# Performance work log

Measured on AMD Instinct MI355X. Metric: run time of the kernel, lower is better.

## Reference

```python
import jax, jax.numpy as jnp
import numpy as np

EPS = 1e-6
ALPHA = 0.2  # LeakyReLU negative slope


def layer_norm(x, g, b):
    mu = jnp.mean(x, axis=-1, keepdims=True)
    var = jnp.mean(jnp.square(x - mu), axis=-1, keepdims=True)
    return (x - mu) * jax.lax.rsqrt(var + EPS) * g + b


def graph_attention(x, bias, W, a_src, a_dst):
    # x: [B,N,D], bias: [B,N,N], W: [D, H*Dh], a_src/a_dst: [H, Dh]
    B, N, D = x.shape
    H, Dh = a_src.shape
    h = jnp.einsum('bnd,dhk->bhnk', x, W.reshape(D, H, Dh))  # [B,H,N,Dh]
    s = jnp.einsum('bhnk,hk->bhn', h, a_src)                 # source term
    t = jnp.einsum('bhnk,hk->bhn', h, a_dst)                 # target term
    e = jax.nn.leaky_relu(s[:, :, :, None] + t[:, :, None, :], ALPHA)
    e = e + bias[:, None, :, :]                              # graph mask/bias
    attn = jax.nn.softmax(e, axis=-1)                        # [B,H,N,N]
    out = jnp.einsum('bhij,bhjk->bhik', attn, h)             # [B,H,N,Dh]
    return out.transpose(0, 2, 1, 3).reshape(B, N, H * Dh)


def setup_inputs() -> dict:
    key = jax.random.key(0)
    ks = jax.random.split(key, 8)
    B, N, D, H = 2, 2048, 512, 8
    Dh = D // H
    sc = 1.0 / np.sqrt(D)
    return {
        'x': jax.random.normal(ks[0], (B, N, D), jnp.float32),
        'bias': jax.random.normal(ks[1], (B, N, N), jnp.float32),
        'W1': jax.random.normal(ks[2], (D, D), jnp.float32) * sc,
        'a_src1': jax.random.normal(ks[3], (H, Dh), jnp.float32) * sc,
        'a_dst1': jax.random.normal(ks[4], (H, Dh), jnp.float32) * sc,
        'g1': jnp.ones((D,), jnp.float32),
        'b1': jnp.zeros((D,), jnp.float32),
        'W2': jax.random.normal(ks[5], (D, D), jnp.float32) * sc,
        'a_src2': jax.random.normal(ks[6], (1, D), jnp.float32) * sc,
        'a_dst2': jax.random.normal(ks[7], (1, D), jnp.float32) * sc,
        'g2': jnp.ones((D,), jnp.float32),
        'b2': jnp.zeros((D,), jnp.float32),
    }


def reference(x, bias, W1, a_src1, a_dst1, g1, b1, W2, a_src2, a_dst2, g2, b2):
    # dropout is identity in eval mode
    attn_in = layer_norm(x, g1, b1)
    attn = graph_attention(attn_in, bias, W1, a_src1, a_dst1) + x
    attn_in2 = layer_norm(attn, g2, b2)
    out = graph_attention(attn_in2, bias, W2, a_src2, a_dst2) + attn
    return out
```

## Files before the change

kernel.cpp:

```cpp
#include <hip/hip_runtime.h>
#include <math.h>

#define NB 2
#define NN 2048
#define DD 512
#define L2E 1.44269504088896340736f

typedef __attribute__((ext_vector_type(8))) short short8;
typedef __attribute__((ext_vector_type(4))) float f32x4;

__device__ __forceinline__ unsigned short f2bf(float x) {
  union { float f; unsigned u; } a;
  a.f = x;
  unsigned r = a.u + 0x7FFF + ((a.u >> 16) & 1);
  return (unsigned short)(r >> 16);
}
__device__ __forceinline__ float bf2f(unsigned short u) {
  union { unsigned u; float f; } a;
  a.u = ((unsigned)u) << 16;
  return a.f;
}
__device__ __forceinline__ unsigned cvtpk(float lo, float hi) {
  unsigned r;
  asm("v_cvt_pk_bf16_f32 %0, %1, %2" : "=v"(r) : "v"(lo), "v"(hi));
  return r;
}
__device__ __forceinline__ uint2 exp4pk(float e0, float e1, float e2, float e3) {
  float p0, p1, p2, p3;
  uint2 d;
  asm("v_exp_f32 %2, %6\n\t"
      "v_exp_f32 %3, %7\n\t"
      "v_exp_f32 %4, %8\n\t"
      "v_exp_f32 %5, %9\n\t"
      "v_cvt_pk_bf16_f32 %0, %2, %3\n\t"
      "v_cvt_pk_bf16_f32 %1, %4, %5"
      : "=&v"(d.x), "=&v"(d.y), "=&v"(p0), "=&v"(p1), "=&v"(p2), "=&v"(p3)
      : "v"(e0), "v"(e1), "v"(e2), "v"(e3));
  return d;
}

__device__ __forceinline__ float waveReduceSum(float v) {
#pragma unroll
  for (int o = 32; o; o >>= 1) v += __shfl_down(v, o, 64);
  return v;
}
__device__ __forceinline__ float blockReduceSum(float v, float* red4) {
  int tid = threadIdx.x;
  __syncthreads();
  v = waveReduceSum(v);
  if ((tid & 63) == 0) red4[tid >> 6] = v;
  __syncthreads();
  return red4[0] + red4[1] + red4[2] + red4[3];
}

__global__ __launch_bounds__(256) void prep_kernel(
    const float* __restrict__ W1, const float* __restrict__ W2,
    unsigned short* __restrict__ WT1, unsigned short* __restrict__ WT2,
    const float* __restrict__ as1, const float* __restrict__ ad1,
    float* __restrict__ vs1, float* __restrict__ vd1,
    const float* __restrict__ as2, const float* __restrict__ ad2,
    float* __restrict__ vs2, float* __restrict__ vd2) {
  __shared__ float tile[64][65];
  int bid = blockIdx.x;
  int t = threadIdx.x;
  if (bid < 128) {
    const float* W = (bid & 64) ? W2 : W1;
    unsigned short* WT = (bid & 64) ? WT2 : WT1;
    int r = bid & 63;
    int kt = (r >> 3) * 64, ct = (r & 7) * 64;
#pragma unroll
    for (int u = 0; u < 16; u++) {
      int lin = t + u * 256;
      int kl = lin >> 6, cl = lin & 63;
      tile[kl][cl] = W[(size_t)(kt + kl) * DD + ct + cl];
    }
    __syncthreads();
#pragma unroll
    for (int u = 0; u < 16; u++) {
      int lin = t + u * 256;
      int cl = lin >> 6, kl = lin & 63;
      WT[(size_t)(ct + cl) * DD + kt + kl] = f2bf(tile[kl][cl]);
    }
  } else {
    int idx = bid - 128;
    int slot = idx >> 3, dch = idx & 7;
    const float *W, *as, *ad;
    float *vs, *vd;
    int Dh, hoff;
    if (slot < 8) {
      W = W1; as = as1 + slot * 64; ad = ad1 + slot * 64;
      vs = vs1 + (size_t)slot * DD; vd = vd1 + (size_t)slot * DD;
      Dh = 64; hoff = slot * 64;
    } else {
      W = W2; as = as2; ad = ad2; vs = vs2; vd = vd2;
      Dh = 512; hoff = 0;
    }
    int dl = t >> 2, kq = t & 3;
    int d = dch * 64 + dl;
    int kn = Dh >> 2;
    const float* wr = W + (size_t)d * DD + hoff + kq * kn;
    const float* asp = as + kq * kn;
    const float* adp = ad + kq * kn;
    float s = 0.f, dd2 = 0.f;
    for (int k = 0; k < kn; k++) {
      float wv = wr[k];
      s += wv * asp[k];
      dd2 += wv * adp[k];
    }
    s += __shfl_xor(s, 1);
    s += __shfl_xor(s, 2);
    dd2 += __shfl_xor(dd2, 1);
    dd2 += __shfl_xor(dd2, 2);
    if (kq == 0) {
      vs[d] = s;
      vd[d] = dd2;
    }
  }
}

__global__ __launch_bounds__(256) void lnst_kernel(
    const float* __restrict__ x, const float* __restrict__ g,
    const float* __restrict__ bb, unsigned short* __restrict__ y,
    const float* __restrict__ vs, const float* __restrict__ vd,
    float* __restrict__ sOut, float* __restrict__ tOut, int HN) {
  __shared__ float red4[4];
  __shared__ float lnS[512];
  int row = blockIdx.x;
  int t = threadIdx.x;
  const float* xr = x + (size_t)row * DD;
  float2 v = *(const float2*)&xr[2 * t];
  float s = blockReduceSum(v.x + v.y, red4);
  float mu = s * (1.0f / 512.0f);
  float d0 = v.x - mu, d1 = v.y - mu;
  float ss = blockReduceSum(d0 * d0 + d1 * d1, red4);
  float rstd = rsqrtf(ss * (1.0f / 512.0f) + 1e-6f);
  float2 gg = *(const float2*)&g[2 * t];
  float2 bv = *(const float2*)&bb[2 * t];
  float n0 = d0 * rstd * gg.x + bv.x;
  float n1 = d1 * rstd * gg.y + bv.y;
  ushort2 o;
  o.x = f2bf(n0);
  o.y = f2bf(n1);
  *(ushort2*)&y[(size_t)row * DD + 2 * t] = o;
  lnS[2 * t] = n0;
  lnS[2 * t + 1] = n1;
  __syncthreads();
  int wv = t >> 6, l = t & 63;
  int b = row >> 11, n = row & (NN - 1);
  float4 x0 = *(const float4*)&lnS[l * 8];
  float4 x1 = *(const float4*)&lnS[l * 8 + 4];
  for (int h = wv; h < HN; h += 4) {
    const float* vsr = vs + (size_t)h * DD + l * 8;
    const float* vdr = vd + (size_t)h * DD + l * 8;
    float4 a0 = *(const float4*)vsr, a1 = *(const float4*)(vsr + 4);
    float4 c0 = *(const float4*)vdr, c1 = *(const float4*)(vdr + 4);
    float ps = x0.x * a0.x + x0.y * a0.y + x0.z * a0.z + x0.w * a0.w +
               x1.x * a1.x + x1.y * a1.y + x1.z * a1.z + x1.w * a1.w;
    float pd = x0.x * c0.x + x0.y * c0.y + x0.z * c0.z + x0.w * c0.w +
               x1.x * c1.x + x1.y * c1.y + x1.z * c1.z + x1.w * c1.w;
#pragma unroll
    for (int o2 = 32; o2; o2 >>= 1) {
      ps += __shfl_xor(ps, o2);
      pd += __shfl_xor(pd, o2);
    }
    if (l == 0) {
      sOut[((size_t)b * HN + h) * NN + n] = ps * L2E;
      tOut[((size_t)b * HN + h) * NN + n] = pd * L2E;
    }
  }
}

__global__ __launch_bounds__(256) void gemm_kernel(const unsigned short* __restrict__ A,
                                                   const unsigned short* __restrict__ BT,
                                                   unsigned short* __restrict__ hbT) {
  __shared__ float accL[4][16][65];
  int t = threadIdx.x, w = t >> 6, l = t & 63;
  int li = l & 15, lg = l >> 4;
  int R0 = blockIdx.x * 16;
  int c0 = blockIdx.y * 64;
  const unsigned short* ar = A + (size_t)(R0 + li) * DD + w * 128 + lg * 8;
  const unsigned short* br = BT + (size_t)(c0 + li) * DD + w * 128 + lg * 8;
  f32x4 acc[4] = {};
#pragma unroll
  for (int k0 = 0; k0 < 128; k0 += 32) {
    short8 af = *(const short8*)(ar + k0);
#pragma unroll
    for (int f = 0; f < 4; f++) {
      short8 bf = *(const short8*)(br + (size_t)f * 16 * DD + k0);
      acc[f] = __builtin_amdgcn_mfma_f32_16x16x32_bf16(af, bf, acc[f], 0, 0, 0);
    }
  }
#pragma unroll
  for (int f = 0; f < 4; f++)
#pragma unroll
    for (int r = 0; r < 4; r++) accL[w][lg * 4 + r][f * 16 + li] = acc[f][r];
  __syncthreads();
  int b = R0 >> 11, jT = (R0 & (NN - 1)) >> 4;
#pragma unroll
  for (int u = 0; u < 2; u++) {
    int idx = t + u * 256;
    int f = idx >> 7;
    int rem = idx & 127;
    int cl = rem >> 3, jlp = rem & 7;
    int cc = f * 16 + cl;
    float v0 = accL[0][2 * jlp][cc] + accL[1][2 * jlp][cc] + accL[2][2 * jlp][cc] +
               accL[3][2 * jlp][cc];
    float v1 = accL[0][2 * jlp + 1][cc] + accL[1][2 * jlp + 1][cc] +
               accL[2][2 * jlp + 1][cc] + accL[3][2 * jlp + 1][cc];
    size_t off = (((size_t)(b * (DD / 64) + blockIdx.y) * (NN / 16)) + jT) * 1024 +
                 f * 256 + cl * 16 + jlp * 2;
    *(unsigned*)(hbT + off) = cvtpk(v0, v1);
  }
}

__global__ __launch_bounds__(512) void pvh_kernel(
    const unsigned short* __restrict__ hbT, const float* __restrict__ bias,
    const float* __restrict__ sArr, const float* __restrict__ tArr,
    const float* __restrict__ res, float* __restrict__ out) {
  __shared__ unsigned short Pl[8][2][1024];
  int t = threadIdx.x, w = t >> 6, l = t & 63;
  int li = l & 15, lg = l >> 4;
  int i0g = blockIdx.x * 16;
  int b = i0g >> 11, i0 = i0g & (NN - 1);
  size_t bhN = (size_t)(b * 8 + w) * NN;
  const float* trow = tArr + bhN;

  int rs = l >> 3, js = (l & 7) * 8, jc = l & 7;
  int wchunk = ((jc & 4) | ((jc & 3) ^ (rs & 3))) * 8;
  float sv[2];
  sv[0] = sArr[bhN + i0 + rs];
  sv[1] = sArr[bhN + i0 + 8 + rs];
  const float* bb0 = bias + ((size_t)b * NN + i0 + rs) * NN;
  const float* bb1 = bb0 + (size_t)8 * NN;

  const unsigned short* vbase =
      hbT + ((size_t)(b * 8 + w) * (NN / 16)) * 1024 + (lg >> 1) * 1024 + li * 16 +
      (lg & 1) * 8;
  int ra0 = li * 64 + (lg ^ (li & 3)) * 8;
  int ra1 = ra0 + 32;

  union { short8 v; unsigned short q[8]; } ones;
#pragma unroll
  for (int k = 0; k < 8; k++) ones.q[k] = 0x3F80;

  f32x4 acc[4] = {};
  f32x4 accS = {0.f, 0.f, 0.f, 0.f};

  auto loadTB = [&](int j, float4& t0, float4& t1, float4& b0a, float4& b0b,
                    float4& b1a, float4& b1b) {
    t0 = *(const float4*)&trow[j + js];
    t1 = *(const float4*)&trow[j + js + 4];
    b0a = *(const float4*)&bb0[j + js];
    b0b = *(const float4*)&bb0[j + js + 4];
    b1a = *(const float4*)&bb1[j + js];
    b1b = *(const float4*)&bb1[j + js + 4];
  };
  auto computeP = [&](const float4& t0, const float4& t1, const float4& b0a,
                      const float4& b0b, const float4& b1a, const float4& b1b, int pb) {
#pragma unroll
    for (int u = 0; u < 2; u++) {
      const float4& ba = u ? b1a : b0a;
      const float4& bc = u ? b1b : b0b;
      int row = u * 8 + rs;
      float e0 = sv[u] + t0.x, e1 = sv[u] + t0.y;
      float e2 = sv[u] + t0.z, e3 = sv[u] + t0.w;
      float e4 = sv[u] + t1.x, e5 = sv[u] + t1.y;
      float e6 = sv[u] + t1.z, e7 = sv[u] + t1.w;
      e0 = fmaf(ba.x, L2E, fmaxf(e0, 0.2f * e0));
      e1 = fmaf(ba.y, L2E, fmaxf(e1, 0.2f * e1));
      e2 = fmaf(ba.z, L2E, fmaxf(e2, 0.2f * e2));
      e3 = fmaf(ba.w, L2E, fmaxf(e3, 0.2f * e3));
      e4 = fmaf(bc.x, L2E, fmaxf(e4, 0.2f * e4));
      e5 = fmaf(bc.y, L2E, fmaxf(e5, 0.2f * e5));
      e6 = fmaf(bc.z, L2E, fmaxf(e6, 0.2f * e6));
      e7 = fmaf(bc.w, L2E, fmaxf(e7, 0.2f * e7));
      uint2 d0 = exp4pk(e0, e1, e2, e3);
      uint2 d1 = exp4pk(e4, e5, e6, e7);
      uint4 dd;
      dd.x = d0.x; dd.y = d0.y; dd.z = d1.x; dd.w = d1.y;
      *(uint4*)&Pl[w][pb][row * 64 + wchunk] = dd;
    }
  };

  float4 tA0, tA1, bA0, bA1, bA2, bA3;

  loadTB(0, tA0, tA1, bA0, bA1, bA2, bA3);
  computeP(tA0, tA1, bA0, bA1, bA2, bA3, 0);
  loadTB(64, tA0, tA1, bA0, bA1, bA2, bA3);

  int buf = 0;
  for (int jt = 0; jt < NN; jt += 64) {
    const unsigned short* vp = vbase + (size_t)jt * 64;
    short8 v0 = *(const short8*)(vp + 0);
    short8 v1 = *(const short8*)(vp + 256);
    short8 v2 = *(const short8*)(vp + 512);
    short8 v3 = *(const short8*)(vp + 768);
    short8 v4 = *(const short8*)(vp + 2048);
    short8 v5 = *(const short8*)(vp + 2304);
    short8 v6 = *(const short8*)(vp + 2560);
    short8 v7 = *(const short8*)(vp + 2816);
    short8 a0 = *(const short8*)&Pl[w][buf][ra0];
    short8 a1 = *(const short8*)&Pl[w][buf][ra1];
    if (jt + 64 < NN) {
      float4 n0 = tA0, n1 = tA1, m0 = bA0, m1 = bA1, m2 = bA2, m3 = bA3;
      int jn = (jt + 128 < NN) ? (jt + 128) : 0;
      loadTB(jn, tA0, tA1, bA0, bA1, bA2, bA3);
      computeP(n0, n1, m0, m1, m2, m3, buf ^ 1);
    }
    __builtin_amdgcn_s_setprio(1);
    accS = __builtin_amdgcn_mfma_f32_16x16x32_bf16(a0, ones.v, accS, 0, 0, 0);
    acc[0] = __builtin_amdgcn_mfma_f32_16x16x32_bf16(a0, v0, acc[0], 0, 0, 0);
    acc[1] = __builtin_amdgcn_mfma_f32_16x16x32_bf16(a0, v1, acc[1], 0, 0, 0);
    acc[2] = __builtin_amdgcn_mfma_f32_16x16x32_bf16(a0, v2, acc[2], 0, 0, 0);
    acc[3] = __builtin_amdgcn_mfma_f32_16x16x32_bf16(a0, v3, acc[3], 0, 0, 0);
    accS = __builtin_amdgcn_mfma_f32_16x16x32_bf16(a1, ones.v, accS, 0, 0, 0);
    acc[0] = __builtin_amdgcn_mfma_f32_16x16x32_bf16(a1, v4, acc[0], 0, 0, 0);
    acc[1] = __builtin_amdgcn_mfma_f32_16x16x32_bf16(a1, v5, acc[1], 0, 0, 0);
    acc[2] = __builtin_amdgcn_mfma_f32_16x16x32_bf16(a1, v6, acc[2], 0, 0, 0);
    acc[3] = __builtin_amdgcn_mfma_f32_16x16x32_bf16(a1, v7, acc[3], 0, 0, 0);
    __builtin_amdgcn_s_setprio(0);
    buf ^= 1;
  }

#pragma unroll
  for (int r = 0; r < 4; r++) {
    float inv = 1.0f / accS[r];
    size_t ix = ((size_t)b * NN + i0 + lg * 4 + r) * DD + w * 64 + li;
#pragma unroll
    for (int f = 0; f < 4; f++) out[ix + f * 16] = acc[f][r] * inv + res[ix + f * 16];
  }
}

template <int HN, int CCH>
__global__ __launch_bounds__(256) void pv_kernel(
    const unsigned short* __restrict__ hbT, const float* __restrict__ bias,
    const float* __restrict__ sArr, const float* __restrict__ tArr,
    const float* __restrict__ res, float* __restrict__ out) {
  constexpr int DH = DD / HN;
  __shared__ unsigned short Pl[4][2][1024];
  __shared__ float accL[4][16][33];
  __shared__ float sLa[4][16];
  int t = threadIdx.x, w = t >> 6, l = t & 63;
  int li = l & 15, lg = l >> 4;
  int i0 = blockIdx.x * 16;
  int ck = blockIdx.y, bh = blockIdx.z;
  int h = bh % HN, b = bh / HN;
  int c0 = h * DH + ck * (CCH * 64);
  size_t bhN = (size_t)bh * NN;
  const float* trow = tArr + bhN;

  int rs = l >> 3, js = (l & 7) * 8, jc = l & 7;
  int wchunk = ((jc & 4) | ((jc & 3) ^ (rs & 3))) * 8;
  float sv[2];
  sv[0] = sArr[bhN + i0 + rs];
  sv[1] = sArr[bhN + i0 + 8 + rs];
  const float* bb0 = bias + ((size_t)b * NN + i0 + rs) * NN;
  const float* bb1 = bb0 + (size_t)8 * NN;

  const unsigned short* vbase =
      hbT + ((size_t)(b * (DD / 64) + (c0 >> 6)) * (NN / 16)) * 1024 +
      (lg >> 1) * 1024 + li * 16 + (lg & 1) * 8;
  int ra0 = li * 64 + (lg ^ (li & 3)) * 8;
  int ra1 = ra0 + 32;

  union { short8 v; unsigned short q[8]; } ones;
#pragma unroll
  for (int k = 0; k < 8; k++) ones.q[k] = 0x3F80;

  const int jbeg = w * (NN / 4), jend = jbeg + NN / 4;
  f32x4 acc[CCH][4] = {};
  f32x4 accS = {0.f, 0.f, 0.f, 0.f};

  auto loadTB = [&](int j, float4& t0, float4& t1, float4& b0a, float4& b0b,
                    float4& b1a, float4& b1b) {
    t0 = *(const float4*)&trow[j + js];
    t1 = *(const float4*)&trow[j + js + 4];
    b0a = *(const float4*)&bb0[j + js];
    b0b = *(const float4*)&bb0[j + js + 4];
    b1a = *(const float4*)&bb1[j + js];
    b1b = *(const float4*)&bb1[j + js + 4];
  };
  auto computeP = [&](const float4& t0, const float4& t1, const float4& b0a,
                      const float4& b0b, const float4& b1a, const float4& b1b, int pb) {
#pragma unroll
    for (int u = 0; u < 2; u++) {
      const float4& ba = u ? b1a : b0a;
      const float4& bc = u ? b1b : b0b;
      int row = u * 8 + rs;
      float e0 = sv[u] + t0.x, e1 = sv[u] + t0.y;
      float e2 = sv[u] + t0.z, e3 = sv[u] + t0.w;
      float e4 = sv[u] + t1.x, e5 = sv[u] + t1.y;
      float e6 = sv[u] + t1.z, e7 = sv[u] + t1.w;
      e0 = fmaf(ba.x, L2E, fmaxf(e0, 0.2f * e0));
      e1 = fmaf(ba.y, L2E, fmaxf(e1, 0.2f * e1));
      e2 = fmaf(ba.z, L2E, fmaxf(e2, 0.2f * e2));
      e3 = fmaf(ba.w, L2E, fmaxf(e3, 0.2f * e3));
      e4 = fmaf(bc.x, L2E, fmaxf(e4, 0.2f * e4));
      e5 = fmaf(bc.y, L2E, fmaxf(e5, 0.2f * e5));
      e6 = fmaf(bc.z, L2E, fmaxf(e6, 0.2f * e6));
      e7 = fmaf(bc.w, L2E, fmaxf(e7, 0.2f * e7));
      uint2 d0 = exp4pk(e0, e1, e2, e3);
      uint2 d1 = exp4pk(e4, e5, e6, e7);
      uint4 dd;
      dd.x = d0.x; dd.y = d0.y; dd.z = d1.x; dd.w = d1.y;
      *(uint4*)&Pl[w][pb][row * 64 + wchunk] = dd;
    }
  };

  float4 tA0, tA1, bA0, bA1, bA2, bA3;

  loadTB(jbeg, tA0, tA1, bA0, bA1, bA2, bA3);
  computeP(tA0, tA1, bA0, bA1, bA2, bA3, 0);
  loadTB(jbeg + 64, tA0, tA1, bA0, bA1, bA2, bA3);

  int buf = 0;
  for (int jt = jbeg; jt < jend; jt += 64) {
    short8 a0 = *(const short8*)&Pl[w][buf][ra0];
    short8 a1 = *(const short8*)&Pl[w][buf][ra1];
    if (jt + 64 < jend) {
      float4 n0 = tA0, n1 = tA1, m0 = bA0, m1 = bA1, m2 = bA2, m3 = bA3;
      int jn = (jt + 128 < jend) ? (jt + 128) : jbeg;
      loadTB(jn, tA0, tA1, bA0, bA1, bA2, bA3);
      computeP(n0, n1, m0, m1, m2, m3, buf ^ 1);
    }
    __builtin_amdgcn_s_setprio(1);
    accS = __builtin_amdgcn_mfma_f32_16x16x32_bf16(a0, ones.v, accS, 0, 0, 0);
    accS = __builtin_amdgcn_mfma_f32_16x16x32_bf16(a1, ones.v, accS, 0, 0, 0);
#pragma unroll
    for (int cc = 0; cc < CCH; cc++) {
      const unsigned short* vp =
          vbase + (size_t)cc * ((NN / 16) * 1024) + (size_t)jt * 64;
      short8 v0 = *(const short8*)(vp + 0);
      short8 v1 = *(const short8*)(vp + 256);
      short8 v2 = *(const short8*)(vp + 512);
      short8 v3 = *(const short8*)(vp + 768);
      acc[cc][0] = __builtin_amdgcn_mfma_f32_16x16x32_bf16(a0, v0, acc[cc][0], 0, 0, 0);
      acc[cc][1] = __builtin_amdgcn_mfma_f32_16x16x32_bf16(a0, v1, acc[cc][1], 0, 0, 0);
      acc[cc][2] = __builtin_amdgcn_mfma_f32_16x16x32_bf16(a0, v2, acc[cc][2], 0, 0, 0);
      acc[cc][3] = __builtin_amdgcn_mfma_f32_16x16x32_bf16(a0, v3, acc[cc][3], 0, 0, 0);
      short8 v4 = *(const short8*)(vp + 2048);
      short8 v5 = *(const short8*)(vp + 2304);
      short8 v6 = *(const short8*)(vp + 2560);
      short8 v7 = *(const short8*)(vp + 2816);
      acc[cc][0] = __builtin_amdgcn_mfma_f32_16x16x32_bf16(a1, v4, acc[cc][0], 0, 0, 0);
      acc[cc][1] = __builtin_amdgcn_mfma_f32_16x16x32_bf16(a1, v5, acc[cc][1], 0, 0, 0);
      acc[cc][2] = __builtin_amdgcn_mfma_f32_16x16x32_bf16(a1, v6, acc[cc][2], 0, 0, 0);
      acc[cc][3] = __builtin_amdgcn_mfma_f32_16x16x32_bf16(a1, v7, acc[cc][3], 0, 0, 0);
    }
    __builtin_amdgcn_s_setprio(0);
    buf ^= 1;
  }

  if (li == 0) {
#pragma unroll
    for (int r = 0; r < 4; r++) sLa[w][lg * 4 + r] = accS[r];
  }
#pragma unroll
  for (int g = 0; g < 2 * CCH; g++) {
    int cc = g >> 1, half = g & 1;
#pragma unroll
    for (int f = 0; f < 2; f++)
#pragma unroll
      for (int r = 0; r < 4; r++)
        accL[w][lg * 4 + r][f * 16 + li] = acc[cc][half * 2 + f][r];
    __syncthreads();
    {
      int rr = t >> 4, cp = (t & 15) * 2;
      float S = sLa[0][rr] + sLa[1][rr] + sLa[2][rr] + sLa[3][rr];
      float inv = 1.0f / S;
      float2 O = {0.f, 0.f};
#pragma unroll
      for (int w2 = 0; w2 < 4; w2++) {
        O.x += accL[w2][rr][cp];
        O.y += accL[w2][rr][cp + 1];
      }
      size_t ix = ((size_t)b * NN + i0 + rr) * DD + c0 + cc * 64 + half * 32 + cp;
      float2 rv = *(const float2*)&res[ix];
      float2 ov = {O.x * inv + rv.x, O.y * inv + rv.y};
      *(float2*)&out[ix] = ov;
    }
    __syncthreads();
  }
}

extern "C" void kernel_launch(void* const* d_in, const int* in_sizes, int n_in,
                              void* d_out, int out_size, void* d_ws, size_t ws_size,
                              hipStream_t stream) {
  const float* x = (const float*)d_in[0];
  const float* bias = (const float*)d_in[1];
  const float* W1 = (const float*)d_in[2];
  const float* asrc1 = (const float*)d_in[3];
  const float* adst1 = (const float*)d_in[4];
  const float* g1 = (const float*)d_in[5];
  const float* b1 = (const float*)d_in[6];
  const float* W2 = (const float*)d_in[7];
  const float* asrc2 = (const float*)d_in[8];
  const float* adst2 = (const float*)d_in[9];
  const float* g2 = (const float*)d_in[10];
  const float* b2 = (const float*)d_in[11];
  float* out = (float*)d_out;
  float* ws = (float*)d_ws;

  const size_t RC = (size_t)NB * NN * DD;
  float* attnBuf = ws;
  unsigned short* lnB = (unsigned short*)(ws + RC);
  unsigned short* hbT = (unsigned short*)(ws + RC + RC / 2);
  unsigned short* WT1 = (unsigned short*)(ws + 2 * RC);
  unsigned short* WT2 = WT1 + (size_t)DD * DD;
  float* vs1 = (float*)(WT2 + (size_t)DD * DD);
  float* vd1 = vs1 + 8 * DD;
  float* vs2 = vd1 + 8 * DD;
  float* vd2 = vs2 + DD;
  float* sBuf = vd2 + DD;
  float* tBuf = sBuf + 16 * NN;

  const int rows = NB * NN;

  hipLaunchKernelGGL(prep_kernel, dim3(128 + 72), dim3(256), 0, stream, W1, W2, WT1, WT2,
                     asrc1, adst1, vs1, vd1, asrc2, adst2, vs2, vd2);

  hipLaunchKernelGGL(lnst_kernel, dim3(rows), dim3(256), 0, stream, x, g1, b1, lnB, vs1, vd1,
                     sBuf, tBuf, 8);
  hipLaunchKernelGGL(gemm_kernel, dim3(256, 8), dim3(256), 0, stream, lnB, WT1, hbT);
  hipLaunchKernelGGL(pvh_kernel, dim3(256), dim3(512), 0, stream, hbT, bias, sBuf, tBuf, x,
                     attnBuf);

  hipLaunchKernelGGL(lnst_kernel, dim3(rows), dim3(256), 0, stream, attnBuf, g2, b2, lnB, vs2,
                     vd2, sBuf, tBuf, 1);
  hipLaunchKernelGGL(gemm_kernel, dim3(256, 8), dim3(256), 0, stream, lnB, WT2, hbT);
  hipLaunchKernelGGL((pv_kernel<1, 4>), dim3(128, 2, 2), dim3(256), 0, stream, hbT, bias,
                     sBuf, tBuf, attnBuf, out);
}
```

Baseline: 160.3 us.

## Split pvh key range across two wave groups with LDS merge

The multi-head attention-times-V kernel now launches 1024 threads per block, with two groups of 8 waves each handling half of the key dimension for every head. Partial output accumulators and softmax denominators from the second half are written to shared memory and added by the first half before normalization and the residual add. This doubles the resident waves per block to give more latency hiding on a 256-block grid, at the cost of a 64KB shared buffer, two barriers, and the register limit imposed by 1024-thread blocks. The P tile layout in LDS is also changed to a row-split indexing.

```diff
diff --git a/kernel.cpp b/kernel.cpp
--- a/kernel.cpp
+++ b/kernel.cpp
@@ -213,16 +213,18 @@
   }
 }
 
-__global__ __launch_bounds__(512) void pvh_kernel(
+__global__ __launch_bounds__(1024) void pvh_kernel(
     const unsigned short* __restrict__ hbT, const float* __restrict__ bias,
     const float* __restrict__ sArr, const float* __restrict__ tArr,
     const float* __restrict__ res, float* __restrict__ out) {
-  __shared__ unsigned short Pl[8][2][1024];
+  __shared__ __align__(16) unsigned char smem[65536];
+  unsigned short (*Pl)[2][1024] = (unsigned short (*)[2][1024])smem;
   int t = threadIdx.x, w = t >> 6, l = t & 63;
+  int h = w & 7, jh = w >> 3;
   int li = l & 15, lg = l >> 4;
   int i0g = blockIdx.x * 16;
   int b = i0g >> 11, i0 = i0g & (NN - 1);
-  size_t bhN = (size_t)(b * 8 + w) * NN;
+  size_t bhN = (size_t)(b * 8 + h) * NN;
   const float* trow = tArr + bhN;
 
   int rs = l >> 3, js = (l & 7) * 8, jc = l & 7;
@@ -234,7 +236,7 @@
   const float* bb1 = bb0 + (size_t)8 * NN;
 
   const unsigned short* vbase =
-      hbT + ((size_t)(b * 8 + w) * (NN / 16)) * 1024 + (lg >> 1) * 1024 + li * 16 +
+      hbT + ((size_t)(b * 8 + h) * (NN / 16)) * 1024 + (lg >> 1) * 1024 + li * 16 +
       (lg & 1) * 8;
   int ra0 = li * 64 + (lg ^ (li & 3)) * 8;
   int ra1 = ra0 + 32;
@@ -244,6 +246,155 @@
   for (int k = 0; k < 8; k++) ones.q[k] = 0x3F80;
 
   f32x4 acc[4] = {};
+  f32x4 accS = {0.f, 0.f, 0.f, 0.f};
+
+  auto loadTB = [&](int j, float4& t0, float4& t1, float4& b0a, float4& b0b,
+                    float4& b1a, float4& b1b) {
+    t0 = *(const float4*)&trow[j + js];
+    t1 = *(const float4*)&trow[j + js + 4];
+    b0a = *(const float4*)&bb0[j + js];
+    b0b = *(const float4*)&bb0[j + js + 4];
+    b1a = *(const float4*)&bb1[j + js];
+    b1b = *(const float4*)&bb1[j + js + 4];
+  };
+  auto computeP = [&](const float4& t0, const float4& t1, const float4& b0a,
+                      const float4& b0b, const float4& b1a, const float4& b1b, int pb) {
+#pragma unroll
+    for (int u = 0; u < 2; u++) {
+      const float4& ba = u ? b1a : b0a;
+      const float4& bc = u ? b1b : b0b;
+      int row = u * 8 + rs;
+      float e0 = sv[u] + t0.x, e1 = sv[u] + t0.y;
+      float e2 = sv[u] + t0.z, e3 = sv[u] + t0.w;
+      float e4 = sv[u] + t1.x, e5 = sv[u] + t1.y;
+      float e6 = sv[u] + t1.z, e7 = sv[u] + t1.w;
+      e0 = fmaf(ba.x, L2E, fmaxf(e0, 0.2f * e0));
+      e1 = fmaf(ba.y, L2E, fmaxf(e1, 0.2f * e1));
+      e2 = fmaf(ba.z, L2E, fmaxf(e2, 0.2f * e2));
+      e3 = fmaf(ba.w, L2E, fmaxf(e3, 0.2f * e3));
+      e4 = fmaf(bc.x, L2E, fmaxf(e4, 0.2f * e4));
+      e5 = fmaf(bc.y, L2E, fmaxf(e5, 0.2f * e5));
+      e6 = fmaf(bc.z, L2E, fmaxf(e6, 0.2f * e6));
+      e7 = fmaf(bc.w, L2E, fmaxf(e7, 0.2f * e7));
+      uint2 d0 = exp4pk(e0, e1, e2, e3);
+      uint2 d1 = exp4pk(e4, e5, e6, e7);
+      uint4 dd;
+      dd.x = d0.x; dd.y = d0.y; dd.z = d1.x; dd.w = d1.y;
+      *(uint4*)&Pl[w][pb][rs * 64 + u * 512 + wchunk] = dd;
+    }
+  };
+
+  const int jbeg = jh * (NN / 2), jend = jbeg + NN / 2;
+  float4 tA0, tA1, bA0, bA1, bA2, bA3;
+
+  loadTB(jbeg, tA0, tA1, bA0, bA1, bA2, bA3);
+  computeP(tA0, tA1, bA0, bA1, bA2, bA3, 0);
+  loadTB(jbeg + 64, tA0, tA1, bA0, bA1, bA2, bA3);
+
+  int buf = 0;
+  for (int jt = jbeg; jt < jend; jt += 64) {
+    const unsigned short* vp = vbase + (size_t)jt * 64;
+    short8 v0 = *(const short8*)(vp + 0);
+    short8 v1 = *(const short8*)(vp + 256);
+    short8 v2 = *(const short8*)(vp + 512);
+    short8 v3 = *(const short8*)(vp + 768);
+    short8 v4 = *(const short8*)(vp + 2048);
+    short8 v5 = *(const short8*)(vp + 2304);
+    short8 v6 = *(const short8*)(vp + 2560);
+    short8 v7 = *(const short8*)(vp + 2816);
+    short8 a0 = *(const short8*)&Pl[w][buf][(li & 7) * 64 + (li >> 3) * 512 +
+                                            ((lg ^ (li & 3)) * 8)];
+    short8 a1 = *(const short8*)&Pl[w][buf][(li & 7) * 64 + (li >> 3) * 512 + 32 +
+                                            ((lg ^ (li & 3)) * 8)];
+    if (jt + 64 < jend) {
+      float4 n0 = tA0, n1 = tA1, m0 = bA0, m1 = bA1, m2 = bA2, m3 = bA3;
+      int jn = (jt + 128 < jend) ? (jt + 128) : jbeg;
+      loadTB(jn, tA0, tA1, bA0, bA1, bA2, bA3);
+      computeP(n0, n1, m0, m1, m2, m3, buf ^ 1);
+    }
+    __builtin_amdgcn_s_setprio(1);
+    accS = __builtin_amdgcn_mfma_f32_16x16x32_bf16(a0, ones.v, accS, 0, 0, 0);
+    acc[0] = __builtin_amdgcn_mfma_f32_16x16x32_bf16(a0, v0, acc[0], 0, 0, 0);
+    acc[1] = __builtin_amdgcn_mfma_f32_16x16x32_bf16(a0, v1, acc[1], 0, 0, 0);
+    acc[2] = __builtin_amdgcn_mfma_f32_16x16x32_bf16(a0, v2, acc[2], 0, 0, 0);
+    acc[3] = __builtin_amdgcn_mfma_f32_16x16x32_bf16(a0, v3, acc[3], 0, 0, 0);
+    accS = __builtin_amdgcn_mfma_f32_16x16x32_bf16(a1, ones.v, accS, 0, 0, 0);
+    acc[0] = __builtin_amdgcn_mfma_f32_16x16x32_bf16(a1, v4, acc[0], 0, 0, 0);
+    acc[1] = __builtin_amdgcn_mfma_f32_16x16x32_bf16(a1, v5, acc[1], 0, 0, 0);
+    acc[2] = __builtin_amdgcn_mfma_f32_16x16x32_bf16(a1, v6, acc[2], 0, 0, 0);
+    acc[3] = __builtin_amdgcn_mfma_f32_16x16x32_bf16(a1, v7, acc[3], 0, 0, 0);
+    __builtin_amdgcn_s_setprio(0);
+    buf ^= 1;
+  }
+
+  __syncthreads();
+  float* mAcc = (float*)smem;
+  float* mS = (float*)(smem + 8 * 16 * 68 * 4);
+  if (jh == 1) {
+#pragma unroll
+    for (int f = 0; f < 4; f++)
+#pragma unroll
+      for (int r = 0; r < 4; r++)
+        mAcc[((size_t)h * 16 + lg * 4 + r) * 68 + f * 16 + li] = acc[f][r];
+    if (li == 0) {
+#pragma unroll
+      for (int r = 0; r < 4; r++) mS[h * 16 + lg * 4 + r] = accS[r];
+    }
+  }
+  __syncthreads();
+  if (jh == 0) {
+#pragma unroll
+    for (int r = 0; r < 4; r++) {
+      float S = accS[r] + mS[h * 16 + lg * 4 + r];
+      float inv = 1.0f / S;
+      size_t ix = ((size_t)b * NN + i0 + lg * 4 + r) * DD + h * 64 + li;
+#pragma unroll
+      for (int f = 0; f < 4; f++) {
+        float O = acc[f][r] + mAcc[((size_t)h * 16 + lg * 4 + r) * 68 + f * 16 + li];
+        out[ix + f * 16] = O * inv + res[ix + f * 16];
+      }
+    }
+  }
+}
+
+template <int HN, int CCH>
+__global__ __launch_bounds__(256) void pv_kernel(
+    const unsigned short* __restrict__ hbT, const float* __restrict__ bias,
+    const float* __restrict__ sArr, const float* __restrict__ tArr,
+    const float* __restrict__ res, float* __restrict__ out) {
+  constexpr int DH = DD / HN;
+  __shared__ unsigned short Pl[4][2][1024];
+  __shared__ float accL[4][16][33];
+  __shared__ float sLa[4][16];
+  int t = threadIdx.x, w = t >> 6, l = t & 63;
+  int li = l & 15, lg = l >> 4;
+  int i0 = blockIdx.x * 16;
+  int ck = blockIdx.y, bh = blockIdx.z;
+  int h = bh % HN, b = bh / HN;
+  int c0 = h * DH + ck * (CCH * 64);
+  size_t bhN = (size_t)bh * NN;
+  const float* trow = tArr + bhN;
+
+  int rs = l >> 3, js = (l & 7) * 8, jc = l & 7;
+  int wchunk = ((jc & 4) | ((jc & 3) ^ (rs & 3))) * 8;
+  float sv[2];
+  sv[0] = sArr[bhN + i0 + rs];
+  sv[1] = sArr[bhN + i0 + 8 + rs];
+  const float* bb0 = bias + ((size_t)b * NN + i0 + rs) * NN;
+  const float* bb1 = bb0 + (size_t)8 * NN;
+
+  const unsigned short* vbase =
+      hbT + ((size_t)(b * (DD / 64) + (c0 >> 6)) * (NN / 16)) * 1024 +
+      (lg >> 1) * 1024 + li * 16 + (lg & 1) * 8;
+  int ra0 = li * 64 + (lg ^ (li & 3)) * 8;
+  int ra1 = ra0 + 32;
+
+  union { short8 v; unsigned short q[8]; } ones;
+#pragma unroll
+  for (int k = 0; k < 8; k++) ones.q[k] = 0x3F80;
+
+  const int jbeg = w * (NN / 4), jend = jbeg + NN / 4;
+  f32x4 acc[CCH][4] = {};
   f32x4 accS = {0.f, 0.f, 0.f, 0.f};
 
   auto loadTB = [&](int j, float4& t0, float4& t1, float4& b0a, float4& b0b,
@@ -284,131 +435,6 @@
 
   float4 tA0, tA1, bA0, bA1, bA2, bA3;
 
-  loadTB(0, tA0, tA1, bA0, bA1, bA2, bA3);
-  computeP(tA0, tA1, bA0, bA1, bA2, bA3, 0);
-  loadTB(64, tA0, tA1, bA0, bA1, bA2, bA3);
-
-  int buf = 0;
-  for (int jt = 0; jt < NN; jt += 64) {
-    const unsigned short* vp = vbase + (size_t)jt * 64;
-    short8 v0 = *(const short8*)(vp + 0);
-    short8 v1 = *(const short8*)(vp + 256);
-    short8 v2 = *(const short8*)(vp + 512);
-    short8 v3 = *(const short8*)(vp + 768);
-    short8 v4 = *(const short8*)(vp + 2048);
-    short8 v5 = *(const short8*)(vp + 2304);
-    short8 v6 = *(const short8*)(vp + 2560);
-    short8 v7 = *(const short8*)(vp + 2816);
-    short8 a0 = *(const short8*)&Pl[w][buf][ra0];
-    short8 a1 = *(const short8*)&Pl[w][buf][ra1];
-    if (jt + 64 < NN) {
-      float4 n0 = tA0, n1 = tA1, m0 = bA0, m1 = bA1, m2 = bA2, m3 = bA3;
-      int jn = (jt + 128 < NN) ? (jt + 128) : 0;
-      loadTB(jn, tA0, tA1, bA0, bA1, bA2, bA3);
-      computeP(n0, n1, m0, m1, m2, m3, buf ^ 1);
-    }
-    __builtin_amdgcn_s_setprio(1);
-    accS = __builtin_amdgcn_mfma_f32_16x16x32_bf16(a0, ones.v, accS, 0, 0, 0);
-    acc[0] = __builtin_amdgcn_mfma_f32_16x16x32_bf16(a0, v0, acc[0], 0, 0, 0);
-    acc[1] = __builtin_amdgcn_mfma_f32_16x16x32_bf16(a0, v1, acc[1], 0, 0, 0);
-    acc[2] = __builtin_amdgcn_mfma_f32_16x16x32_bf16(a0, v2, acc[2], 0, 0, 0);
-    acc[3] = __builtin_amdgcn_mfma_f32_16x16x32_bf16(a0, v3, acc[3], 0, 0, 0);
-    accS = __builtin_amdgcn_mfma_f32_16x16x32_bf16(a1, ones.v, accS, 0, 0, 0);
-    acc[0] = __builtin_amdgcn_mfma_f32_16x16x32_bf16(a1, v4, acc[0], 0, 0, 0);
-    acc[1] = __builtin_amdgcn_mfma_f32_16x16x32_bf16(a1, v5, acc[1], 0, 0, 0);
-    acc[2] = __builtin_amdgcn_mfma_f32_16x16x32_bf16(a1, v6, acc[2], 0, 0, 0);
-    acc[3] = __builtin_amdgcn_mfma_f32_16x16x32_bf16(a1, v7, acc[3], 0, 0, 0);
-    __builtin_amdgcn_s_setprio(0);
-    buf ^= 1;
-  }
-
-#pragma unroll
-  for (int r = 0; r < 4; r++) {
-    float inv = 1.0f / accS[r];
-    size_t ix = ((size_t)b * NN + i0 + lg * 4 + r) * DD + w * 64 + li;
-#pragma unroll
-    for (int f = 0; f < 4; f++) out[ix + f * 16] = acc[f][r] * inv + res[ix + f * 16];
-  }
-}
-
-template <int HN, int CCH>
-__global__ __launch_bounds__(256) void pv_kernel(
-    const unsigned short* __restrict__ hbT, const float* __restrict__ bias,
-    const float* __restrict__ sArr, const float* __restrict__ tArr,
-    const float* __restrict__ res, float* __restrict__ out) {
-  constexpr int DH = DD / HN;
-  __shared__ unsigned short Pl[4][2][1024];
-  __shared__ float accL[4][16][33];
-  __shared__ float sLa[4][16];
-  int t = threadIdx.x, w = t >> 6, l = t & 63;
-  int li = l & 15, lg = l >> 4;
-  int i0 = blockIdx.x * 16;
-  int ck = blockIdx.y, bh = blockIdx.z;
-  int h = bh % HN, b = bh / HN;
-  int c0 = h * DH + ck * (CCH * 64);
-  size_t bhN = (size_t)bh * NN;
-  const float* trow = tArr + bhN;
-
-  int rs = l >> 3, js = (l & 7) * 8, jc = l & 7;
-  int wchunk = ((jc & 4) | ((jc & 3) ^ (rs & 3))) * 8;
-  float sv[2];
-  sv[0] = sArr[bhN + i0 + rs];
-  sv[1] = sArr[bhN + i0 + 8 + rs];
-  const float* bb0 = bias + ((size_t)b * NN + i0 + rs) * NN;
-  const float* bb1 = bb0 + (size_t)8 * NN;
-
-  const unsigned short* vbase =
-      hbT + ((size_t)(b * (DD / 64) + (c0 >> 6)) * (NN / 16)) * 1024 +
-      (lg >> 1) * 1024 + li * 16 + (lg & 1) * 8;
-  int ra0 = li * 64 + (lg ^ (li & 3)) * 8;
-  int ra1 = ra0 + 32;
-
-  union { short8 v; unsigned short q[8]; } ones;
-#pragma unroll
-  for (int k = 0; k < 8; k++) ones.q[k] = 0x3F80;
-
-  const int jbeg = w * (NN / 4), jend = jbeg + NN / 4;
-  f32x4 acc[CCH][4] = {};
-  f32x4 accS = {0.f, 0.f, 0.f, 0.f};
-
-  auto loadTB = [&](int j, float4& t0, float4& t1, float4& b0a, float4& b0b,
-                    float4& b1a, float4& b1b) {
-    t0 = *(const float4*)&trow[j + js];
-    t1 = *(const float4*)&trow[j + js + 4];
-    b0a = *(const float4*)&bb0[j + js];
-    b0b = *(const float4*)&bb0[j + js + 4];
-    b1a = *(const float4*)&bb1[j + js];
-    b1b = *(const float4*)&bb1[j + js + 4];
-  };
-  auto computeP = [&](const float4& t0, const float4& t1, const float4& b0a,
-                      const float4& b0b, const float4& b1a, const float4& b1b, int pb) {
-#pragma unroll
-    for (int u = 0; u < 2; u++) {
-      const float4& ba = u ? b1a : b0a;
-      const float4& bc = u ? b1b : b0b;
-      int row = u * 8 + rs;
-      float e0 = sv[u] + t0.x, e1 = sv[u] + t0.y;
-      float e2 = sv[u] + t0.z, e3 = sv[u] + t0.w;
-      float e4 = sv[u] + t1.x, e5 = sv[u] + t1.y;
-      float e6 = sv[u] + t1.z, e7 = sv[u] + t1.w;
-      e0 = fmaf(ba.x, L2E, fmaxf(e0, 0.2f * e0));
-      e1 = fmaf(ba.y, L2E, fmaxf(e1, 0.2f * e1));
-      e2 = fmaf(ba.z, L2E, fmaxf(e2, 0.2f * e2));
-      e3 = fmaf(ba.w, L2E, fmaxf(e3, 0.2f * e3));
-      e4 = fmaf(bc.x, L2E, fmaxf(e4, 0.2f * e4));
-      e5 = fmaf(bc.y, L2E, fmaxf(e5, 0.2f * e5));
-      e6 = fmaf(bc.z, L2E, fmaxf(e6, 0.2f * e6));
-      e7 = fmaf(bc.w, L2E, fmaxf(e7, 0.2f * e7));
-      uint2 d0 = exp4pk(e0, e1, e2, e3);
-      uint2 d1 = exp4pk(e4, e5, e6, e7);
-      uint4 dd;
-      dd.x = d0.x; dd.y = d0.y; dd.z = d1.x; dd.w = d1.y;
-      *(uint4*)&Pl[w][pb][row * 64 + wchunk] = dd;
-    }
-  };
-
-  float4 tA0, tA1, bA0, bA1, bA2, bA3;
-
   loadTB(jbeg, tA0, tA1, bA0, bA1, bA2, bA3);
   computeP(tA0, tA1, bA0, bA1, bA2, bA3, 0);
   loadTB(jbeg + 64, tA0, tA1, bA0, bA1, bA2, bA3);
@@ -522,7 +548,7 @@
   hipLaunchKernelGGL(lnst_kernel, dim3(rows), dim3(256), 0, stream, x, g1, b1, lnB, vs1, vd1,
                      sBuf, tBuf, 8);
   hipLaunchKernelGGL(gemm_kernel, dim3(256, 8), dim3(256), 0, stream, lnB, WT1, hbT);
-  hipLaunchKernelGGL(pvh_kernel, dim3(256), dim3(512), 0, stream, hbT, bias, sBuf, tBuf, x,
+  hipLaunchKernelGGL(pvh_kernel, dim3(256), dim3(1024), 0, stream, hbT, bias, sBuf, tBuf, x,
                      attnBuf);
 
   hipLaunchKernelGGL(lnst_kernel, dim3(rows), dim3(256), 0, stream, attnBuf, g2, b2, lnB, vs2,
```

After: 174.0 us. 1.09x slower.
